# Kernel tuning notes

Hardware: AMD Instinct MI355X
Metric: run time of the kernel (lower is better)

The kernel has to match this reference:

```python
import jax, jax.numpy as jnp
import numpy as np

SQRT_HALF = 0.7071067811865476
DILATIONS = [3 ** (i % 4) for i in range(8)]  # [1,3,9,27,1,3,9,27]


def conv1d(x, w, b, dilation=1):
    # x: [B, Cin, L], w: [Cout, Cin, K], 'same' padding
    out = jax.lax.conv_general_dilated(
        x, w, window_strides=(1,), padding='SAME',
        rhs_dilation=(dilation,),
        dimension_numbers=('NCH', 'OIH', 'NCH'))
    return out + b[None, :, None]


def encoder(x, enc_start_w, enc_start_b, glu_w, glu_b, enc_end_w, enc_end_b):
    # EncoderAny (eval mode -> dropout is identity)
    h = conv1d(x, enc_start_w, enc_start_b)                  # [B, mid, N]
    for i in range(len(DILATIONS)):
        g = conv1d(h, glu_w[i], glu_b[i], dilation=DILATIONS[i])  # [B, 2*mid, N]
        a, b = jnp.split(g, 2, axis=1)
        h = (h + a * jax.nn.sigmoid(b)) * SQRT_HALF           # GLU + residual
    out = conv1d(h, enc_end_w, enc_end_b)                     # [B, 2*d, N]
    K, V = jnp.split(out, 2, axis=1)                          # each [B, d, N]
    return K, V


def reference(in_s, in_t, c_t,
              enc_start_w, enc_start_b, glu_w, glu_b, enc_end_w, enc_end_b,
              wc_pre, w_pre, b_pre, wc_post, w_post, b_post):
    # ---- encoder: source -> K, V ----
    K_s, V_s = encoder(in_s, enc_start_w, enc_start_b, glu_w, glu_b,
                       enc_end_w, enc_end_b)                  # [B, d, N] each
    d = K_s.shape[1]

    # ---- pre-decoder: target + speaker code -> Q ----
    h_t = in_t + jnp.einsum('bc,cd->bd', c_t, wc_pre)[:, :, None]  # [B, D, T]
    Q_t = conv1d(h_t, w_pre, b_pre)                           # [B, d, T]

    # ---- custom attention: softmax over SOURCE axis (dim=1) ----
    scores = jnp.einsum('bdn,bdt->bnt', K_s, Q_t) / jnp.sqrt(
        jnp.asarray(d, dtype=K_s.dtype))                      # [B, N, T]
    A = jax.nn.softmax(scores, axis=1)                        # softmax over N
    R = jnp.einsum('bdn,bnt->bdt', V_s, A)                    # [B, d, T]

    # concat with Q (dropout p=0.9 in training; eval/deterministic -> identity)
    R = jnp.concatenate([R, Q_t], axis=1)                     # [B, 2d, T]

    # ---- post-decoder: attended features + speaker code -> y ----
    h_r = R + jnp.einsum('bc,cd->bd', c_t, wc_post)[:, :, None]
    y = conv1d(h_r, w_post, b_post)                           # [B, D, T]
    return y, A


def setup_inputs() -> dict:
    key = jax.random.key(0)
    ks = jax.random.split(key, 16)
    B, D, N, T = 16, 240, 2048, 2048
    mid, d, C = 512, 512, 8
    L = len(DILATIONS)

    def w(k, shape, fan_in):
        return (jax.random.normal(k, shape, dtype=jnp.float32)
                / jnp.sqrt(jnp.asarray(fan_in, jnp.float32)))

    return {
        'in_s': jax.random.normal(ks[0], (B, D, N), dtype=jnp.float32),
        'in_t': jax.random.normal(ks[1], (B, D, T), dtype=jnp.float32),
        'c_t': jax.random.normal(ks[2], (B, C), dtype=jnp.float32),
        'enc_start_w': w(ks[3], (mid, D, 1), D),
        'enc_start_b': jnp.zeros((mid,), jnp.float32),
        'glu_w': w(ks[4], (L, 2 * mid, mid, 5), mid * 5),
        'glu_b': jnp.zeros((L, 2 * mid), jnp.float32),
        'enc_end_w': w(ks[5], (2 * d, mid, 1), mid),
        'enc_end_b': jnp.zeros((2 * d,), jnp.float32),
        'wc_pre': w(ks[6], (C, D), C),
        'w_pre': w(ks[7], (d, D, 1), D),
        'b_pre': jnp.zeros((d,), jnp.float32),
        'wc_post': w(ks[8], (C, 2 * d), C),
        'w_post': w(ks[9], (D, 2 * d, 1), 2 * d),
        'b_post': jnp.zeros((D,), jnp.float32),
    }
```

## Files before the change

kernel.cpp:

```cpp
#include <hip/hip_runtime.h>
#include <cstdint>
#include <cstddef>

typedef unsigned short u16;
typedef __attribute__((ext_vector_type(8))) short short8;
typedef __attribute__((ext_vector_type(4))) float f32x4;

static constexpr int BB = 16, DIN = 240, NN = 2048, TT = 2048;
static constexpr long long Y_SIZE = (long long)BB * DIN * TT;
static constexpr float SQRT_HALF_F = 0.70710678118654752440f;
static constexpr int HPAD = 64;
static constexpr int HROWS = NN + 2 * HPAD;

#define DEVI __device__ __forceinline__

DEVI u16 f2bf(float f) {
    unsigned u = __builtin_bit_cast(unsigned, f);
    u += 0x7FFFu + ((u >> 16) & 1u);
    return (u16)(u >> 16);
}
DEVI float bf2f(u16 h) {
    unsigned u = ((unsigned)h) << 16;
    return __builtin_bit_cast(float, u);
}

DEVI void gld16(const void* g, const void* l) {
    __builtin_amdgcn_global_load_lds(
        (const __attribute__((address_space(1))) unsigned int*)g,
        (__attribute__((address_space(3))) unsigned int*)l, 16, 0, 0);
}

DEVI int glu_perm(int g) {
    int tile = g >> 8, r = g & 255;
    int wcq = r >> 6, r2 = r & 63;
    int n = r2 >> 4, fr = r2 & 15;
    return tile * 128 + wcq * 32 + (n >> 1) * 16 + fr + (n & 1) * 512;
}

struct GemmP {
    const u16* A; long long a_bstride; int lda;
    const u16* Bw; long long b_bstride; long long b_tapstride; int ldb;
    int ntaps; int shift0; int dshift; int Kt; int ks_log2;
    void* out; long long o_bstride; int ldc;
    const float* bias; int bias_bstride;
    float scale;
    int store_ncols;
};

#define FENCE() asm volatile("" ::: "memory")
#define SBAR()  do { FENCE(); __builtin_amdgcn_s_barrier(); FENCE(); } while (0)
#define PH_WAIT() do { asm volatile("s_waitcnt lgkmcnt(0)" ::: "memory"); \
                       __builtin_amdgcn_sched_barrier(0); } while (0)

template <int OUTK>
__global__ __launch_bounds__(512, 2)
void gemm256(GemmP p, int tilesM, int tilesN) {
    __shared__ __align__(16) u16 As[2][256 * 64];
    __shared__ __align__(16) u16 Bs[2][256 * 64];
    const int tid = threadIdx.x;
    const int lane = tid & 63;
    const int wv = tid >> 6;
    const int wr = wv >> 2, wcq = wv & 3;
    const int fr = lane & 15, fq = lane >> 4;

    const int nwg = gridDim.x;
    int widx = (blockIdx.x & 7) * (nwg >> 3) + (blockIdx.x >> 3);
    const int mt = widx % tilesM; widx /= tilesM;
    const int nt = widx % tilesN;
    const int bz = widx / tilesN;
    const int n0 = mt * 256, c0 = nt * 256;

    const int lda = p.lda, ldb = p.ldb;
    const u16* Abase = p.A + (long long)bz * p.a_bstride;
    const u16* Bbase = p.Bw + (long long)bz * p.b_bstride;
    const int kmask = (1 << p.ks_log2) - 1;
    const int tot = p.ntaps << p.ks_log2;

    f32x4 acc[8][4];
#pragma unroll
    for (int m = 0; m < 8; ++m)
#pragma unroll
        for (int n = 0; n < 4; ++n) acc[m][n] = (f32x4){0.f, 0.f, 0.f, 0.f};

    const int srow = lane >> 3, sslot = lane & 7;
    const int js = (sslot ^ srow) << 3;
    const int sr0 = wv * 16 + srow;

    const long long sA8 = 8LL * lda, sAh = 128LL * lda;
    const long long sB8 = 8LL * ldb, sBh = 128LL * ldb;
    const long long dAtap = (long long)p.dshift * lda - (long long)kmask * 64;
    const long long dBtap = p.b_tapstride - (long long)kmask * 64;

    auto aAddr = [&](int t) -> const u16* {
        int tap = t >> p.ks_log2;
        return Abase + (long long)(n0 + p.shift0 + tap * p.dshift + sr0) * lda
               + ((t & kmask) << 6) + js;
    };
    auto bAddr = [&](int t) -> const u16* {
        int tap = t >> p.ks_log2;
        return Bbase + (long long)tap * p.b_tapstride
               + (long long)(c0 + sr0) * ldb + ((t & kmask) << 6) + js;
    };

    u16* uA = &As[0][wv * 1024];
    u16* uB = &Bs[0][wv * 1024];

    {
        const u16* a0 = aAddr(0);
        gld16(a0, uA);              gld16(a0 + sA8, uA + 512);
        gld16(a0 + sAh, uA + 8192); gld16(a0 + sAh + sA8, uA + 8192 + 512);
        const u16* b0 = bAddr(0);
        gld16(b0, uB);              gld16(b0 + sB8, uB + 512);
        gld16(b0 + sBh, uB + 8192); gld16(b0 + sBh + sB8, uB + 8192 + 512);
        const u16* b1 = bAddr(1);
        gld16(b1, uB + 16384);              gld16(b1 + sB8, uB + 16384 + 512);
        gld16(b1 + sBh, uB + 16384 + 8192); gld16(b1 + sBh + sB8, uB + 16384 + 8192 + 512);
    }
    const u16* aP = aAddr(1);
    const u16* bP = bAddr(2);
    asm volatile("s_waitcnt vmcnt(4)" ::: "memory");
    __builtin_amdgcn_s_barrier();
    FENCE();

    const int aoff0 = (wr * 128 + fr) * 64 + ((fq ^ (fr & 7)) << 3);
    const int aoff1 = (wr * 128 + fr) * 64 + (((4 + fq) ^ (fr & 7)) << 3);
    const int boff0 = (wcq * 64 + fr) * 64 + ((fq ^ (fr & 7)) << 3);
    const int boff1 = (wcq * 64 + fr) * 64 + (((4 + fq) ^ (fr & 7)) << 3);

    short8 af[4][2], bf0[2][2], bf1[2][2];

#define READ_AQ(MQ)                                                            \
    _Pragma("unroll")                                                          \
    for (int mi = 0; mi < 4; ++mi) {                                           \
        af[mi][0] = *(const short8*)&Ab[aoff0 + ((MQ) * 64 + mi * 16) * 64];   \
        af[mi][1] = *(const short8*)&Ab[aoff1 + ((MQ) * 64 + mi * 16) * 64];   \
    }
#define READ_BQ(BF, NQ)                                                        \
    _Pragma("unroll")                                                          \
    for (int ni = 0; ni < 2; ++ni) {                                           \
        BF[ni][0] = *(const short8*)&Bb[boff0 + ((NQ) * 32 + ni * 16) * 64];   \
        BF[ni][1] = *(const short8*)&Bb[boff1 + ((NQ) * 32 + ni * 16) * 64];   \
    }
#define MFMA_Q(MQ, NQ, BF)                                                     \
    __builtin_amdgcn_s_setprio(1);                                             \
    _Pragma("unroll")                                                          \
    for (int mi = 0; mi < 4; ++mi) {                                           \
        _Pragma("unroll")                                                      \
        for (int ni = 0; ni < 2; ++ni) {                                       \
            _Pragma("unroll")                                                  \
            for (int kk = 0; kk < 2; ++kk)                                     \
                acc[(MQ) * 4 + mi][(NQ) * 2 + ni] =                            \
                    __builtin_amdgcn_mfma_f32_16x16x32_bf16(                   \
                        af[mi][kk], BF[ni][kk],                                \
                        acc[(MQ) * 4 + mi][(NQ) * 2 + ni], 0, 0, 0);           \
        }                                                                      \
    }                                                                          \
    __builtin_amdgcn_s_setprio(0)

#define TILEBODY(BUF_, DO_A_, DO_B_, STEPA_, STEPB_, VM_)                      \
  {                                                                            \
    const u16* Ab = &As[BUF_][0];                                              \
    const u16* Bb = &Bs[BUF_][0];                                              \
                                        \
    READ_AQ(0);                                                                \
    READ_BQ(bf0, 0);                                                           \
    if (DO_A_) { gld16(aP, uA + ((BUF_) ^ 1) * 16384);                         \
                 gld16(aP + sA8, uA + ((BUF_) ^ 1) * 16384 + 512); }           \
    SBAR();                                                                    \
    PH_WAIT();                                                                 \
    MFMA_Q(0, 0, bf0);                                                         \
    SBAR();                                                                    \
                                        \
    READ_BQ(bf1, 1);                                                           \
    if (DO_A_) { gld16(aP + sAh, uA + ((BUF_) ^ 1) * 16384 + 8192);            \
                 gld16(aP + sAh + sA8, uA + ((BUF_) ^ 1) * 16384 + 8192 + 512);\
                 aP += (STEPA_); }                                             \
    SBAR();                                                                    \
    PH_WAIT();                                                                 \
    MFMA_Q(0, 1, bf1);                                                         \
    SBAR();                                                                    \
                                        \
    READ_AQ(1);                                                                \
    if (DO_B_) { gld16(bP, uB + (BUF_) * 16384);                               \
                 gld16(bP + sB8, uB + (BUF_) * 16384 + 512); }                 \
    SBAR();                                                                    \
    PH_WAIT();                                                                 \
    MFMA_Q(1, 1, bf1);                                                         \
    SBAR();                                                                    \
             \
    if (DO_B_) { gld16(bP + sBh, uB + (BUF_) * 16384 + 8192);                  \
                 gld16(bP + sBh + sB8, uB + (BUF_) * 16384 + 8192 + 512);      \
                 bP += (STEPB_); }                                             \
    SBAR();                                                                    \
    MFMA_Q(1, 0, bf0);                                                         \
    if ((VM_) == 4) asm volatile("s_waitcnt vmcnt(4)" ::: "memory");           \
    else if ((VM_) == 0) asm volatile("s_waitcnt vmcnt(0)" ::: "memory");      \
    SBAR();                                                                    \
  }

    int t = 0;
    for (; t + 3 < tot; t += 2) {
        const long long stA1 = (((t + 2) & kmask) != 0) ? 64 : dAtap;
        const long long stA2 = (((t + 3) & kmask) != 0) ? 64 : dAtap;
        const long long stB1 = (((t + 3) & kmask) != 0) ? 64 : dBtap;
        const long long stB2 = (((t + 4) & kmask) != 0) ? 64 : dBtap;
        TILEBODY(0, 1, 1, stA1, stB1, 4);
        TILEBODY(1, 1, 1, stA2, stB2, 4);
    }
    TILEBODY(0, 1, 0, 0, 0, 0);
    TILEBODY(1, 0, 0, 0, 0, -1);
#undef READ_AQ
#undef READ_BQ
#undef MFMA_Q
#undef TILEBODY

    if constexpr (OUTK == 4) {
        const float* bp = p.bias;
#pragma unroll
        for (int m = 0; m < 8; ++m) {
#pragma unroll
            for (int pr = 0; pr < 2; ++pr) {
                int ca = c0 + wcq * 64 + (2 * pr) * 16 + fr;
                int chan = (c0 >> 1) + wcq * 32 + pr * 16 + fr;
                float biasa = bp[ca], biasb = bp[ca + 16];
#pragma unroll
                for (int r = 0; r < 4; ++r) {
                    int row = n0 + wr * 128 + m * 16 + fq * 4 + r;
                    float a = acc[m][2 * pr][r] + biasa;
                    float bq = acc[m][2 * pr + 1][r] + biasb;
                    float sig = 1.f / (1.f + __expf(-bq));
                    float h = bf2f(Abase[(long long)row * lda + chan]);
                    ((u16*)p.out)[(long long)bz * p.o_bstride + (long long)row * p.ldc + chan]
                        = f2bf((h + a * sig) * SQRT_HALF_F);
                }
            }
        }
        return;
    } else {
        const float* bias = p.bias ? p.bias + (long long)bz * p.bias_bstride : nullptr;
#pragma unroll
        for (int m = 0; m < 8; ++m) {
#pragma unroll
            for (int n = 0; n < 4; ++n) {
                int col = c0 + wcq * 64 + n * 16 + fr;
                float cb = (OUTK == 1 && bias) ? bias[col] : 0.f;
#pragma unroll
                for (int r = 0; r < 4; ++r) {
                    int row = n0 + wr * 128 + m * 16 + fq * 4 + r;
                    float v = acc[m][n][r] * p.scale + cb;
                    if (OUTK == 5) v += bias[row];
                    ((u16*)p.out)[(long long)bz * p.o_bstride + (long long)row * p.ldc + col]
                        = f2bf(v);
                }
            }
        }
    }
}

template <int OUTK>
__global__ __launch_bounds__(256, 2)
void gemm_kernel(GemmP p) {
    __shared__ u16 As[128 * 64];
    __shared__ u16 Bs[128 * 64];
    const int tid = threadIdx.x;
    const int lane = tid & 63, wv = tid >> 6;
    const int wr = wv >> 1, wc = wv & 1;
    const int bz = blockIdx.z;
    const int n0 = blockIdx.x * 128;
    const int c0 = blockIdx.y * 128;
    const u16* Abase = p.A + (long long)bz * p.a_bstride;
    const u16* Bbase = p.Bw + (long long)bz * p.b_bstride;

    f32x4 acc[4][4];
#pragma unroll
    for (int i = 0; i < 4; ++i)
#pragma unroll
        for (int j = 0; j < 4; ++j) acc[i][j] = (f32x4){0.f, 0.f, 0.f, 0.f};

    const int ksteps = p.Kt >> 6;
    const int tot = p.ntaps * ksteps;
    const int srow = lane >> 3;
    const int scol = (lane & 7) * 8;
    const int fr = lane & 15;
    const int fk = (lane >> 4) * 8;

    for (int t = 0; t < tot; ++t) {
        const int tap = t / ksteps;
        const int ks = (t - tap * ksteps) << 6;
        const int shift = p.shift0 + tap * p.dshift;
        __syncthreads();
        {
            const u16* asrc = Abase + (long long)(n0 + shift) * p.lda + ks;
#pragma unroll
            for (int c = 0; c < 4; ++c) {
                int chunk = wv * 4 + c;
                int row = chunk * 8 + srow;
                gld16(asrc + (long long)row * p.lda + scol, &As[chunk * 512]);
            }
            const u16* bsrc = Bbase + (long long)tap * p.b_tapstride + (long long)c0 * p.ldb + ks;
#pragma unroll
            for (int c = 0; c < 4; ++c) {
                int chunk = wv * 4 + c;
                int row = chunk * 8 + srow;
                gld16(bsrc + (long long)row * p.ldb + scol, &Bs[chunk * 512]);
            }
        }
        asm volatile("s_waitcnt vmcnt(0)" ::: "memory");
        __syncthreads();
#pragma unroll
        for (int kk = 0; kk < 2; ++kk) {
            short8 af[4], bfr[4];
#pragma unroll
            for (int m = 0; m < 4; ++m) {
                int arow = wr * 64 + m * 16 + fr;
                af[m] = *(const short8*)&As[arow * 64 + kk * 32 + fk];
            }
#pragma unroll
            for (int nn2 = 0; nn2 < 4; ++nn2) {
                int brow = wc * 64 + nn2 * 16 + fr;
                bfr[nn2] = *(const short8*)&Bs[brow * 64 + kk * 32 + fk];
            }
#pragma unroll
            for (int m = 0; m < 4; ++m)
#pragma unroll
                for (int nn2 = 0; nn2 < 4; ++nn2)
                    acc[m][nn2] = __builtin_amdgcn_mfma_f32_16x16x32_bf16(
                        af[m], bfr[nn2], acc[m][nn2], 0, 0, 0);
        }
    }

    const float* bias = p.bias ? p.bias + (long long)bz * p.bias_bstride : nullptr;
#pragma unroll
    for (int m = 0; m < 4; ++m) {
#pragma unroll
        for (int nn2 = 0; nn2 < 4; ++nn2) {
#pragma unroll
            for (int r = 0; r < 4; ++r) {
                int row = n0 + wr * 64 + m * 16 + ((lane >> 4) << 2) + r;
                int col = c0 + wc * 64 + nn2 * 16 + (lane & 15);
                if (col >= p.store_ncols) continue;
                float v = acc[m][nn2][r] * p.scale;
                if (bias) v += bias[col];
                long long off = (OUTK == 0 || OUTK == 1)
                                    ? (long long)row * p.ldc + col
                                    : (long long)col * p.ldc + row;
                long long idx = (long long)bz * p.o_bstride + off;
                if (OUTK == 0 || OUTK == 2) ((float*)p.out)[idx] = v;
                else ((u16*)p.out)[idx] = f2bf(v);
            }
        }
    }
}


__global__ void cvt_glu(const float* src, u16* dst) {
    long long t = (long long)blockIdx.x * blockDim.x + threadIdx.x;
    const long long total = 8LL * 5 * 1024 * 512;
    if (t >= total) return;
    int i = (int)(t % 512); long long r = t / 512;
    int g = (int)(r % 1024); r /= 1024;
    int k = (int)(r % 5); int l = (int)(r / 5);
    int o = glu_perm(g);
    dst[t] = f2bf(src[(((long long)l * 1024 + o) * 512 + i) * 5 + k]);
}

__global__ void perm_bias(const float* gb, float* biasP) {
    int t = blockIdx.x * 256 + threadIdx.x;
    if (t >= 8 * 1024) return;
    int g = t & 1023, l = t >> 10;
    biasP[t] = gb[l * 1024 + glu_perm(g)];
}

__global__ void cvt_pad(const float* src, u16* dst, int Os, int Is, int Od, int Id) {
    long long t = (long long)blockIdx.x * blockDim.x + threadIdx.x;
    if (t >= (long long)Od * Id) return;
    int i = (int)(t % Id); int o = (int)(t / Id);
    float v = (o < Os && i < Is) ? src[(long long)o * Is + i] : 0.f;
    dst[t] = f2bf(v);
}

__global__ void transpose_in(const float* src, u16* dst, int Csrc, int Cdst, int Len) {
    __shared__ float tile[32][33];
    int b = blockIdx.z;
    int n0 = blockIdx.x * 32, c0 = blockIdx.y * 32;
    int tx = threadIdx.x, ty = threadIdx.y;
    int c = c0 + ty, n = n0 + tx;
    float v = 0.f;
    if (c < Csrc) v = src[((long long)b * Csrc + c) * Len + n];
    tile[ty][tx] = v;
    __syncthreads();
    dst[((long long)b * Len + (n0 + ty)) * Cdst + (c0 + tx)] = f2bf(tile[tx][ty]);
}

__global__ void zero_pads(u16* h) {
    long long t = (long long)blockIdx.x * blockDim.x + threadIdx.x;
    const long long total = (long long)BB * 128 * 512;
    if (t >= total) return;
    int c = (int)(t % 512); long long r = t / 512;
    int rr = (int)(r % 128); int b = (int)(r / 128);
    int row = rr < HPAD ? rr : (HROWS - 128 + rr);
    h[((long long)b * HROWS + row) * 512 + c] = 0;
}

__global__ void prebias_kernel(const float* ct, const float* wcpre, const float* wpre,
                               const float* bpre, float* qbias) {
    __shared__ float s[240];
    int b = blockIdx.x; int tid = threadIdx.x;
    if (tid < 240) {
        float a = 0.f;
        for (int c = 0; c < 8; ++c) a += ct[b * 8 + c] * wcpre[c * 240 + tid];
        s[tid] = a;
    }
    __syncthreads();
    for (int o = tid; o < 512; o += 256) {
        float a = bpre[o];
        for (int d0 = 0; d0 < 240; ++d0) a += wpre[o * 240 + d0] * s[d0];
        qbias[b * 512 + o] = a;
    }
}

__global__ void postbias_kernel(const float* ct, const float* wcpost, const float* wpost,
                                const float* bpost, float* ybias) {
    __shared__ float s[1024];
    int b = blockIdx.x; int tid = threadIdx.x;
    for (int e = tid; e < 1024; e += 256) {
        float a = 0.f;
        for (int c = 0; c < 8; ++c) a += ct[b * 8 + c] * wcpost[c * 1024 + e];
        s[e] = a;
    }
    __syncthreads();
    if (tid < 240) {
        float a = bpost[tid];
        for (int e = 0; e < 1024; ++e) a += wpost[tid * 1024 + e] * s[e];
        ybias[b * 240 + tid] = a;
    }
}

__global__ __launch_bounds__(256)
void softmax_rows(const u16* St, u16* AT) {
    int b = blockIdx.y;
    int t = blockIdx.x * 4 + (threadIdx.x >> 6);
    int lane = threadIdx.x & 63;
    const u16* row = St + ((long long)b * TT + t) * NN;
    short8 v[4];
#pragma unroll
    for (int i = 0; i < 4; ++i) v[i] = ((const short8*)row)[i * 64 + lane];
    float f[32];
#pragma unroll
    for (int i = 0; i < 4; ++i)
#pragma unroll
        for (int j = 0; j < 8; ++j) f[i * 8 + j] = bf2f((u16)v[i][j]);
    float m = -3.4e38f;
#pragma unroll
    for (int i = 0; i < 32; ++i) m = fmaxf(m, f[i]);
#pragma unroll
    for (int s = 1; s < 64; s <<= 1) m = fmaxf(m, __shfl_xor(m, s, 64));
    float sum = 0.f;
#pragma unroll
    for (int i = 0; i < 32; ++i) { f[i] = __expf(f[i] - m); sum += f[i]; }
#pragma unroll
    for (int s = 1; s < 64; s <<= 1) sum += __shfl_xor(sum, s, 64);
    float li = 1.f / sum;
    u16* atrow = AT + ((long long)b * TT + t) * NN;
#pragma unroll
    for (int i = 0; i < 4; ++i) {
        short8 pk;
#pragma unroll
        for (int j = 0; j < 8; ++j) pk[j] = (short)f2bf(f[i * 8 + j] * li);
        ((short8*)atrow)[i * 64 + lane] = pk;
    }
}

__global__ void transpose_out(const u16* AT, float* A) {
    __shared__ float tile[32][33];
    int b = blockIdx.z;
    int n0 = blockIdx.x * 32, t0 = blockIdx.y * 32;
    int tx = threadIdx.x, ty = threadIdx.y;
#pragma unroll
    for (int k = 0; k < 4; ++k) {
        int t = t0 + ty + k * 8;
        tile[ty + k * 8][tx] = bf2f(AT[((long long)b * TT + t) * NN + n0 + tx]);
    }
    __syncthreads();
#pragma unroll
    for (int k = 0; k < 4; ++k) {
        int n = n0 + ty + k * 8;
        A[((long long)b * NN + n) * TT + t0 + tx] = tile[tx][ty + k * 8];
    }
}


extern "C" void kernel_launch(void* const* d_in, const int* in_sizes, int n_in,
                              void* d_out, int out_size, void* d_ws, size_t ws_size,
                              hipStream_t stream) {
    const float* in_s        = (const float*)d_in[0];
    const float* in_t        = (const float*)d_in[1];
    const float* c_t         = (const float*)d_in[2];
    const float* enc_start_w = (const float*)d_in[3];
    const float* enc_start_b = (const float*)d_in[4];
    const float* glu_w       = (const float*)d_in[5];
    const float* glu_b       = (const float*)d_in[6];
    const float* enc_end_w   = (const float*)d_in[7];
    const float* enc_end_b   = (const float*)d_in[8];
    const float* wc_pre      = (const float*)d_in[9];
    const float* w_pre       = (const float*)d_in[10];
    const float* b_pre       = (const float*)d_in[11];
    const float* wc_post     = (const float*)d_in[12];
    const float* w_post      = (const float*)d_in[13];
    const float* b_post      = (const float*)d_in[14];

    char* w = (char*)d_ws;
    u16* wglu   = (u16*)w; w += 8LL * 5 * 1024 * 512 * 2;
    u16* wstart = (u16*)w; w += 512LL * 256 * 2;
    u16* wend   = (u16*)w; w += 1024LL * 512 * 2;
    u16* wpre   = (u16*)w; w += 512LL * 256 * 2;
    u16* wpost  = (u16*)w; w += 256LL * 1024 * 2;
    u16* XS     = (u16*)w; w += (long long)BB * NN * 256 * 2;
    u16* XT     = (u16*)w; w += (long long)BB * TT * 256 * 2;
    u16* h0     = (u16*)w; w += (long long)BB * HROWS * 512 * 2;
    u16* h1     = (u16*)w; w += (long long)BB * HROWS * 512 * 2;
    u16* Kb     = (u16*)w; w += (long long)BB * NN * 512 * 2;
    u16* Vb     = (u16*)w; w += (long long)BB * 512 * NN * 2;
    u16* Rc     = (u16*)w; w += (long long)BB * TT * 1024 * 2;
    u16* ATb    = (u16*)w; w += (long long)BB * TT * NN * 2;
    float* qbias = (float*)w; w += 16LL * 512 * 4;
    float* ybias = (float*)w; w += 16LL * 256 * 4;
    float* biasP = (float*)w; w += 8LL * 1024 * 4;
    if ((size_t)(w - (char*)d_ws) > ws_size) return;

    float* yout = (float*)d_out;
    float* Areg = yout + Y_SIZE;
    u16* Sbf = (u16*)Areg;

    cvt_glu<<<(8LL * 5 * 1024 * 512 + 255) / 256, 256, 0, stream>>>(glu_w, wglu);
    perm_bias<<<(8 * 1024 + 255) / 256, 256, 0, stream>>>(glu_b, biasP);
    cvt_pad<<<(512 * 256 + 255) / 256, 256, 0, stream>>>(enc_start_w, wstart, 512, 240, 512, 256);
    cvt_pad<<<(1024 * 512 + 255) / 256, 256, 0, stream>>>(enc_end_w, wend, 1024, 512, 1024, 512);
    cvt_pad<<<(512 * 256 + 255) / 256, 256, 0, stream>>>(w_pre, wpre, 512, 240, 512, 256);
    cvt_pad<<<(256 * 1024 + 255) / 256, 256, 0, stream>>>(w_post, wpost, 240, 1024, 256, 1024);
    transpose_in<<<dim3(NN / 32, 256 / 32, BB), dim3(32, 32), 0, stream>>>(in_s, XS, 240, 256, NN);
    transpose_in<<<dim3(TT / 32, 256 / 32, BB), dim3(32, 32), 0, stream>>>(in_t, XT, 240, 256, TT);
    zero_pads<<<((long long)BB * 128 * 512 + 255) / 256, 256, 0, stream>>>(h0);
    zero_pads<<<((long long)BB * 128 * 512 + 255) / 256, 256, 0, stream>>>(h1);
    prebias_kernel<<<16, 256, 0, stream>>>(c_t, wc_pre, w_pre, b_pre, qbias);
    postbias_kernel<<<16, 256, 0, stream>>>(c_t, wc_post, w_post, b_post, ybias);

    {
        GemmP p{}; p.A = XS; p.a_bstride = (long long)NN * 256; p.lda = 256;
        p.Bw = wstart; p.b_bstride = 0; p.b_tapstride = 0; p.ldb = 256;
        p.ntaps = 1; p.shift0 = 0; p.dshift = 0; p.Kt = 256; p.ks_log2 = 2;
        p.out = h0 + HPAD * 512; p.o_bstride = (long long)HROWS * 512; p.ldc = 512;
        p.bias = enc_start_b; p.bias_bstride = 0; p.scale = 1.f; p.store_ncols = 512;
        gemm256<1><<<8 * 2 * 16, 512, 0, stream>>>(p, 8, 2);
    }

    const int dils[8] = {1, 3, 9, 27, 1, 3, 9, 27};
    u16* hin = h0; u16* hout = h1;
    for (int l = 0; l < 8; ++l) {
        GemmP q{}; q.A = hin + HPAD * 512; q.a_bstride = (long long)HROWS * 512; q.lda = 512;
        q.Bw = wglu + (long long)l * 5 * 1024 * 512; q.b_bstride = 0;
        q.b_tapstride = 1024LL * 512; q.ldb = 512;
        q.ntaps = 5; q.shift0 = -2 * dils[l]; q.dshift = dils[l]; q.Kt = 512; q.ks_log2 = 3;
        q.out = hout + HPAD * 512; q.o_bstride = (long long)HROWS * 512; q.ldc = 512;
        q.bias = biasP + l * 1024; q.bias_bstride = 0; q.scale = 1.f; q.store_ncols = 1024;
        gemm256<4><<<8 * 4 * 16, 512, 0, stream>>>(q, 8, 4);
        u16* tmp = hin; hin = hout; hout = tmp;
    }

    {
        GemmP p{}; p.A = hin + HPAD * 512; p.a_bstride = (long long)HROWS * 512; p.lda = 512;
        p.Bw = wend; p.b_bstride = 0; p.b_tapstride = 0; p.ldb = 512;
        p.ntaps = 1; p.shift0 = 0; p.dshift = 0; p.Kt = 512; p.ks_log2 = 3;
        p.out = Kb; p.o_bstride = (long long)NN * 512; p.ldc = 512;
        p.bias = enc_end_b; p.bias_bstride = 0; p.scale = 1.f; p.store_ncols = 512;
        gemm256<1><<<8 * 2 * 16, 512, 0, stream>>>(p, 8, 2);
    }
    {
        GemmP p{}; p.A = wend + 512LL * 512; p.a_bstride = 0; p.lda = 512;
        p.Bw = hin + HPAD * 512; p.b_bstride = (long long)HROWS * 512; p.b_tapstride = 0; p.ldb = 512;
        p.ntaps = 1; p.shift0 = 0; p.dshift = 0; p.Kt = 512; p.ks_log2 = 3;
        p.out = Vb; p.o_bstride = 512LL * NN; p.ldc = NN;
        p.bias = enc_end_b + 512; p.bias_bstride = 0; p.scale = 1.f; p.store_ncols = NN;
        gemm256<5><<<2 * 8 * 16, 512, 0, stream>>>(p, 2, 8);
    }

    {
        GemmP p{}; p.A = XT; p.a_bstride = (long long)TT * 256; p.lda = 256;
        p.Bw = wpre; p.b_bstride = 0; p.b_tapstride = 0; p.ldb = 256;
        p.ntaps = 1; p.shift0 = 0; p.dshift = 0; p.Kt = 256; p.ks_log2 = 2;
        p.out = Rc + 512; p.o_bstride = (long long)TT * 1024; p.ldc = 1024;
        p.bias = qbias; p.bias_bstride = 512; p.scale = 1.f; p.store_ncols = 512;
        gemm256<1><<<8 * 2 * 16, 512, 0, stream>>>(p, 8, 2);
    }

    {
        GemmP p{}; p.A = Rc + 512; p.a_bstride = (long long)TT * 1024; p.lda = 1024;
        p.Bw = Kb; p.b_bstride = (long long)NN * 512; p.b_tapstride = 0; p.ldb = 512;
        p.ntaps = 1; p.shift0 = 0; p.dshift = 0; p.Kt = 512; p.ks_log2 = 3;
        p.out = Sbf; p.o_bstride = (long long)TT * NN; p.ldc = NN;
        p.bias = nullptr; p.bias_bstride = 0; p.scale = 0.04419417382415922f;
        p.store_ncols = NN;
        gemm256<1><<<8 * 8 * 16, 512, 0, stream>>>(p, 8, 8);
    }

    softmax_rows<<<dim3(TT / 4, BB), 256, 0, stream>>>(Sbf, ATb);
    transpose_out<<<dim3(NN / 32, TT / 32, BB), dim3(32, 8), 0, stream>>>(ATb, Areg);

    {
        GemmP p{}; p.A = ATb; p.a_bstride = (long long)TT * NN; p.lda = NN;
        p.Bw = Vb; p.b_bstride = 512LL * NN; p.b_tapstride = 0; p.ldb = NN;
        p.ntaps = 1; p.shift0 = 0; p.dshift = 0; p.Kt = NN; p.ks_log2 = 5;
        p.out = Rc; p.o_bstride = (long long)TT * 1024; p.ldc = 1024;
        p.bias = nullptr; p.bias_bstride = 0; p.scale = 1.f; p.store_ncols = 512;
        gemm256<1><<<8 * 2 * 16, 512, 0, stream>>>(p, 8, 2);
    }

    {
        GemmP p{}; p.A = Rc; p.a_bstride = (long long)TT * 1024; p.lda = 1024;
        p.Bw = wpost; p.b_bstride = 0; p.b_tapstride = 0; p.ldb = 1024;
        p.ntaps = 1; p.shift0 = 0; p.dshift = 0; p.Kt = 1024; p.ks_log2 = 4;
        p.out = yout; p.o_bstride = (long long)DIN * TT; p.ldc = TT;
        p.bias = ybias; p.bias_bstride = 240; p.scale = 1.f; p.store_ncols = 240;
        gemm_kernel<2><<<dim3(16, 2, 16), 256, 0, stream>>>(p);
    }
}
```

Before: 1.866 ms.

## Restructure gemm256 inner schedule into two phases and route post-decoder GEMM through it

The 256x256 GEMM main loop goes from four barrier-separated quarter phases, each with an explicit LDS wait, to two phases. Each phase preloads A and both B fragment sets into separate registers, then issues two MFMA quarters back to back. This removes most barriers and lgkmcnt waits, at the cost of more fragment registers. The older 128x128 gemm_kernel is deleted, and the post-decoder projection now uses gemm256 with a new transposed fp32 output path with bias. That path pads the 240 output channels to a 256 tile and launches far fewer workgroups (128).

New measurement: 1.780 ms. 4.6% less time.

```diff
diff --git a/kernel.cpp b/kernel.cpp
--- a/kernel.cpp
+++ b/kernel.cpp
@@ -49,8 +49,6 @@
 
 #define FENCE() asm volatile("" ::: "memory")
 #define SBAR()  do { FENCE(); __builtin_amdgcn_s_barrier(); FENCE(); } while (0)
-#define PH_WAIT() do { asm volatile("s_waitcnt lgkmcnt(0)" ::: "memory"); \
-                       __builtin_amdgcn_sched_barrier(0); } while (0)
 
 template <int OUTK>
 __global__ __launch_bounds__(512, 2)
@@ -127,13 +125,13 @@
     const int boff0 = (wcq * 64 + fr) * 64 + ((fq ^ (fr & 7)) << 3);
     const int boff1 = (wcq * 64 + fr) * 64 + (((4 + fq) ^ (fr & 7)) << 3);
 
-    short8 af[4][2], bf0[2][2], bf1[2][2];
-
-#define READ_AQ(MQ)                                                            \
+    short8 af0[4][2], af1[4][2], bf0[2][2], bf1[2][2];
+
+#define READ_AQ(DEST, MQ)                                                      \
     _Pragma("unroll")                                                          \
     for (int mi = 0; mi < 4; ++mi) {                                           \
-        af[mi][0] = *(const short8*)&Ab[aoff0 + ((MQ) * 64 + mi * 16) * 64];   \
-        af[mi][1] = *(const short8*)&Ab[aoff1 + ((MQ) * 64 + mi * 16) * 64];   \
+        DEST[mi][0] = *(const short8*)&Ab[aoff0 + ((MQ) * 64 + mi * 16) * 64]; \
+        DEST[mi][1] = *(const short8*)&Ab[aoff1 + ((MQ) * 64 + mi * 16) * 64]; \
     }
 #define READ_BQ(BF, NQ)                                                        \
     _Pragma("unroll")                                                          \
@@ -141,7 +139,7 @@
         BF[ni][0] = *(const short8*)&Bb[boff0 + ((NQ) * 32 + ni * 16) * 64];   \
         BF[ni][1] = *(const short8*)&Bb[boff1 + ((NQ) * 32 + ni * 16) * 64];   \
     }
-#define MFMA_Q(MQ, NQ, BF)                                                     \
+#define MFMA_Q2(MQ, NQ, AF, BF)                                                \
     __builtin_amdgcn_s_setprio(1);                                             \
     _Pragma("unroll")                                                          \
     for (int mi = 0; mi < 4; ++mi) {                                           \
@@ -151,7 +149,7 @@
             for (int kk = 0; kk < 2; ++kk)                                     \
                 acc[(MQ) * 4 + mi][(NQ) * 2 + ni] =                            \
                     __builtin_amdgcn_mfma_f32_16x16x32_bf16(                   \
-                        af[mi][kk], BF[ni][kk],                                \
+                        AF[mi][kk], BF[ni][kk],                                \
                         acc[(MQ) * 4 + mi][(NQ) * 2 + ni], 0, 0, 0);           \
         }                                                                      \
     }                                                                          \
@@ -161,38 +159,27 @@
   {                                                                            \
     const u16* Ab = &As[BUF_][0];                                              \
     const u16* Bb = &Bs[BUF_][0];                                              \
-                                        \
-    READ_AQ(0);                                                                \
+      \
+    READ_AQ(af0, 0);                                                           \
     READ_BQ(bf0, 0);                                                           \
+    READ_BQ(bf1, 1);                                                           \
     if (DO_A_) { gld16(aP, uA + ((BUF_) ^ 1) * 16384);                         \
-                 gld16(aP + sA8, uA + ((BUF_) ^ 1) * 16384 + 512); }           \
-    SBAR();                                                                    \
-    PH_WAIT();                                                                 \
-    MFMA_Q(0, 0, bf0);                                                         \
-    SBAR();                                                                    \
-                                        \
-    READ_BQ(bf1, 1);                                                           \
-    if (DO_A_) { gld16(aP + sAh, uA + ((BUF_) ^ 1) * 16384 + 8192);            \
+                 gld16(aP + sA8, uA + ((BUF_) ^ 1) * 16384 + 512);             \
+                 gld16(aP + sAh, uA + ((BUF_) ^ 1) * 16384 + 8192);            \
                  gld16(aP + sAh + sA8, uA + ((BUF_) ^ 1) * 16384 + 8192 + 512);\
                  aP += (STEPA_); }                                             \
+    MFMA_Q2(0, 0, af0, bf0);                                                   \
+    MFMA_Q2(0, 1, af0, bf1);                                                   \
     SBAR();                                                                    \
-    PH_WAIT();                                                                 \
-    MFMA_Q(0, 1, bf1);                                                         \
-    SBAR();                                                                    \
-                                        \
-    READ_AQ(1);                                                                \
+                    \
+    READ_AQ(af1, 1);                                                           \
     if (DO_B_) { gld16(bP, uB + (BUF_) * 16384);                               \
-                 gld16(bP + sB8, uB + (BUF_) * 16384 + 512); }                 \
-    SBAR();                                                                    \
-    PH_WAIT();                                                                 \
-    MFMA_Q(1, 1, bf1);                                                         \
-    SBAR();                                                                    \
-             \
-    if (DO_B_) { gld16(bP + sBh, uB + (BUF_) * 16384 + 8192);                  \
+                 gld16(bP + sB8, uB + (BUF_) * 16384 + 512);                   \
+                 gld16(bP + sBh, uB + (BUF_) * 16384 + 8192);                  \
                  gld16(bP + sBh + sB8, uB + (BUF_) * 16384 + 8192 + 512);      \
                  bP += (STEPB_); }                                             \
-    SBAR();                                                                    \
-    MFMA_Q(1, 0, bf0);                                                         \
+    MFMA_Q2(1, 1, af1, bf1);                                                   \
+    MFMA_Q2(1, 0, af1, bf0);                                                   \
     if ((VM_) == 4) asm volatile("s_waitcnt vmcnt(4)" ::: "memory");           \
     else if ((VM_) == 0) asm volatile("s_waitcnt vmcnt(0)" ::: "memory");      \
     SBAR();                                                                    \
@@ -211,7 +198,7 @@
     TILEBODY(1, 0, 0, 0, 0, -1);
 #undef READ_AQ
 #undef READ_BQ
-#undef MFMA_Q
+#undef MFMA_Q2
 #undef TILEBODY
 
     if constexpr (OUTK == 4) {
@@ -236,6 +223,24 @@
             }
         }
         return;
+    } else if constexpr (OUTK == 2) {
+        const float* bias = p.bias + (long long)bz * p.bias_bstride;
+#pragma unroll
+        for (int m = 0; m < 8; ++m) {
+#pragma unroll
+            for (int n = 0; n < 4; ++n) {
+                int col = c0 + wcq * 64 + n * 16 + fr;
+                if (col >= p.store_ncols) continue;
+                float cb = bias[col];
+#pragma unroll
+                for (int r = 0; r < 4; ++r) {
+                    int row = n0 + wr * 128 + m * 16 + fq * 4 + r;
+                    ((float*)p.out)[(long long)bz * p.o_bstride + (long long)col * p.ldc + row]
+                        = acc[m][n][r] * p.scale + cb;
+                }
+            }
+        }
+        return;
     } else {
         const float* bias = p.bias ? p.bias + (long long)bz * p.bias_bstride : nullptr;
 #pragma unroll
@@ -252,101 +257,6 @@
                     ((u16*)p.out)[(long long)bz * p.o_bstride + (long long)row * p.ldc + col]
                         = f2bf(v);
                 }
-            }
-        }
-    }
-}
-
-template <int OUTK>
-__global__ __launch_bounds__(256, 2)
-void gemm_kernel(GemmP p) {
-    __shared__ u16 As[128 * 64];
-    __shared__ u16 Bs[128 * 64];
-    const int tid = threadIdx.x;
-    const int lane = tid & 63, wv = tid >> 6;
-    const int wr = wv >> 1, wc = wv & 1;
-    const int bz = blockIdx.z;
-    const int n0 = blockIdx.x * 128;
-    const int c0 = blockIdx.y * 128;
-    const u16* Abase = p.A + (long long)bz * p.a_bstride;
-    const u16* Bbase = p.Bw + (long long)bz * p.b_bstride;
-
-    f32x4 acc[4][4];
-#pragma unroll
-    for (int i = 0; i < 4; ++i)
-#pragma unroll
-        for (int j = 0; j < 4; ++j) acc[i][j] = (f32x4){0.f, 0.f, 0.f, 0.f};
-
-    const int ksteps = p.Kt >> 6;
-    const int tot = p.ntaps * ksteps;
-    const int srow = lane >> 3;
-    const int scol = (lane & 7) * 8;
-    const int fr = lane & 15;
-    const int fk = (lane >> 4) * 8;
-
-    for (int t = 0; t < tot; ++t) {
-        const int tap = t / ksteps;
-        const int ks = (t - tap * ksteps) << 6;
-        const int shift = p.shift0 + tap * p.dshift;
-        __syncthreads();
-        {
-            const u16* asrc = Abase + (long long)(n0 + shift) * p.lda + ks;
-#pragma unroll
-            for (int c = 0; c < 4; ++c) {
-                int chunk = wv * 4 + c;
-                int row = chunk * 8 + srow;
-                gld16(asrc + (long long)row * p.lda + scol, &As[chunk * 512]);
-            }
-            const u16* bsrc = Bbase + (long long)tap * p.b_tapstride + (long long)c0 * p.ldb + ks;
-#pragma unroll
-            for (int c = 0; c < 4; ++c) {
-                int chunk = wv * 4 + c;
-                int row = chunk * 8 + srow;
-                gld16(bsrc + (long long)row * p.ldb + scol, &Bs[chunk * 512]);
-            }
-        }
-        asm volatile("s_waitcnt vmcnt(0)" ::: "memory");
-        __syncthreads();
-#pragma unroll
-        for (int kk = 0; kk < 2; ++kk) {
-            short8 af[4], bfr[4];
-#pragma unroll
-            for (int m = 0; m < 4; ++m) {
-                int arow = wr * 64 + m * 16 + fr;
-                af[m] = *(const short8*)&As[arow * 64 + kk * 32 + fk];
-            }
-#pragma unroll
-            for (int nn2 = 0; nn2 < 4; ++nn2) {
-                int brow = wc * 64 + nn2 * 16 + fr;
-                bfr[nn2] = *(const short8*)&Bs[brow * 64 + kk * 32 + fk];
-            }
-#pragma unroll
-            for (int m = 0; m < 4; ++m)
-#pragma unroll
-                for (int nn2 = 0; nn2 < 4; ++nn2)
-                    acc[m][nn2] = __builtin_amdgcn_mfma_f32_16x16x32_bf16(
-                        af[m], bfr[nn2], acc[m][nn2], 0, 0, 0);
-        }
-    }
-
-    const float* bias = p.bias ? p.bias + (long long)bz * p.bias_bstride : nullptr;
-#pragma unroll
-    for (int m = 0; m < 4; ++m) {
-#pragma unroll
-        for (int nn2 = 0; nn2 < 4; ++nn2) {
-#pragma unroll
-            for (int r = 0; r < 4; ++r) {
-                int row = n0 + wr * 64 + m * 16 + ((lane >> 4) << 2) + r;
-                int col = c0 + wc * 64 + nn2 * 16 + (lane & 15);
-                if (col >= p.store_ncols) continue;
-                float v = acc[m][nn2][r] * p.scale;
-                if (bias) v += bias[col];
-                long long off = (OUTK == 0 || OUTK == 1)
-                                    ? (long long)row * p.ldc + col
-                                    : (long long)col * p.ldc + row;
-                long long idx = (long long)bz * p.o_bstride + off;
-                if (OUTK == 0 || OUTK == 2) ((float*)p.out)[idx] = v;
-                else ((u16*)p.out)[idx] = f2bf(v);
             }
         }
     }
@@ -621,6 +531,6 @@
         p.ntaps = 1; p.shift0 = 0; p.dshift = 0; p.Kt = 1024; p.ks_log2 = 4;
         p.out = yout; p.o_bstride = (long long)DIN * TT; p.ldc = TT;
         p.bias = ybias; p.bias_bstride = 240; p.scale = 1.f; p.store_ncols = 240;
-        gemm_kernel<2><<<dim3(16, 2, 16), 256, 0, stream>>>(p);
-    }
-}
+        gemm256<2><<<8 * 1 * 16, 512, 0, stream>>>(p, 8, 1);
+    }
+}
```
